# Kernel tuning notes

Measured on AMD Instinct MI355X. Metric: run time of the kernel, lower is better.

The kernel has to match this reference:

```python
import jax, jax.numpy as jnp
import numpy as np

B, S, D, E = 8, 4096, 4096, 64
CAP_FACTOR = 1.1


def setup_inputs() -> dict:
    key = jax.random.key(0)
    k1, k2 = jax.random.split(key)
    x = jax.random.normal(k1, (B, S, D), jnp.float32)
    # original zero-inits the router weight (degenerate routing); use small random
    # weights so top-2 routing is non-trivial. Forward math is identical.
    W = jax.random.normal(k2, (E, D), jnp.float32) * 0.02
    return {"x": x, "W": W}


def reference(x, W):
    b, s, d = x.shape
    e = W.shape[0]
    tokens = b * s
    capacity = int(tokens * CAP_FACTOR * 2 / e)  # static Python int

    # router: logits = x @ W^T (nn.Linear, no bias)
    logits = jnp.einsum('bsd,ed->bse', x, W)
    probs = jax.nn.softmax(logits, axis=-1)

    top2_p, top2_i = jax.lax.top_k(probs, 2)            # [b,s,2]
    top2_pn = top2_p / top2_p.sum(-1, keepdims=True)     # renormalized top-2 probs

    # Flatten the (token, slot) pairs in the same (i,j,k) enumeration order as
    # the reference triple loop; stable argsort reproduces its tie-breaking.
    n2 = tokens * 2
    e_flat = top2_i.reshape(n2)                          # expert id per slot
    p_flat = top2_pn.reshape(n2)                         # prob per slot
    onehot = e_flat[:, None] == jnp.arange(e)[None, :]   # [n2, e] bool

    # per-expert rank of each assigned slot by descending prob (stable)
    pe = jnp.where(onehot, p_flat[:, None], -jnp.inf)    # [n2, e]
    order = jnp.argsort(-pe, axis=0)                     # stable sort, desc prob
    rank = jnp.argsort(order, axis=0)                    # rank of slot within expert
    keep = onehot & (rank < capacity)                    # capacity truncation

    keep = keep.reshape(b, s, 2, e)
    dispatch = keep.any(axis=2).astype(x.dtype)                       # [b,s,e]
    combine = (keep.astype(x.dtype) * top2_pn[..., None]).sum(axis=2)  # [b,s,e]

    # aux loss: uses pre-truncation counts (expert_counts in the loop counts all
    # top-2 assignments, before capacity dropping)
    prob_per_expert = probs.sum(axis=(0, 1)) / tokens
    counts = onehot.sum(axis=0).astype(x.dtype)
    usage = counts / counts.sum()
    aux_loss = (prob_per_expert * usage).sum() * e

    return dispatch, combine, probs, aux_loss
```

## Files before the change

kernel.cpp:

```cpp
#include <hip/hip_runtime.h>
#include <hip/hip_bf16.h>
#include <cstdint>
#include <cstddef>

#define TOKENS   32768
#define DDIM     4096
#define NEXP     64
#define N2       65536
#define CAPACITY 1126

#define WS_WT    0
#define WS_PFLAT (1u << 20)
#define WS_EFLAT ((1u << 20) + 262144u)
#define WS_PSUM  ((1u << 20) + 524288u)
#define WS_CNT   ((1u << 20) + 524288u + 256u)

__global__ void zero_kernel(float* __restrict__ dc, float* __restrict__ psum) {
    int idx = blockIdx.x * blockDim.x + threadIdx.x;
    float4 z = make_float4(0.f, 0.f, 0.f, 0.f);
    const int n4 = (2 * TOKENS * NEXP) / 4;
    for (int i = idx; i < n4; i += gridDim.x * blockDim.x)
        ((float4*)dc)[i] = z;
    if (idx < NEXP) psum[idx] = 0.f;
}

__global__ void transpose_w(const float* __restrict__ W, float* __restrict__ Wt) {
    int idx = blockIdx.x * 256 + threadIdx.x;
    int d = idx >> 6, e = idx & 63;
    Wt[idx] = W[(size_t)e * DDIM + d];
}

__launch_bounds__(256, 2)
__global__ void router_kernel(const float* __restrict__ x, const float* __restrict__ Wt,
                              float* __restrict__ probs_out, float* __restrict__ p_flat,
                              int* __restrict__ e_flat, float* __restrict__ psum) {
    __shared__ __align__(16) float xs[64][68];
    __shared__ __align__(16) float wt[64][68];
    __shared__ __align__(16) float prow[64][68];
    __shared__ float red[256];

    const int tid  = threadIdx.x;
    const int tok0 = blockIdx.x * 64;
    const int ty4  = (tid >> 4) * 4;
    const int tx4  = (tid & 15) * 4;

    float tacc[4][4];
#pragma unroll
    for (int i = 0; i < 4; ++i)
#pragma unroll
        for (int j = 0; j < 4; ++j) tacc[i][j] = 0.f;

    for (int d0 = 0; d0 < DDIM; d0 += 64) {
        __syncthreads();
#pragma unroll
        for (int it = 0; it < 4; ++it) {
            int q   = it * 256 + tid;
            int row = q >> 4;
            int fp  = (q & 15) * 4;
            float4 xv = *(const float4*)&x[(size_t)(tok0 + row) * DDIM + d0 + fp];
            *(float4*)&xs[row][fp] = xv;
            float4 wv = *(const float4*)&Wt[(size_t)(d0 + row) * 64 + fp];
            *(float4*)&wt[row][fp] = wv;
        }
        __syncthreads();

        float cacc[4][4];
#pragma unroll
        for (int i = 0; i < 4; ++i)
#pragma unroll
            for (int j = 0; j < 4; ++j) cacc[i][j] = 0.f;

#pragma unroll 4
        for (int kk = 0; kk < 64; kk += 4) {
            float xr[4][4], wr[4][4];
#pragma unroll
            for (int i = 0; i < 4; ++i)
                *(float4*)xr[i] = *(const float4*)&xs[ty4 + i][kk];
#pragma unroll
            for (int t = 0; t < 4; ++t)
                *(float4*)wr[t] = *(const float4*)&wt[kk + t][tx4];
#pragma unroll
            for (int i = 0; i < 4; ++i)
#pragma unroll
                for (int t = 0; t < 4; ++t)
#pragma unroll
                    for (int j = 0; j < 4; ++j)
                        cacc[i][j] = fmaf(xr[i][t], wr[t][j], cacc[i][j]);
        }
#pragma unroll
        for (int i = 0; i < 4; ++i)
#pragma unroll
            for (int j = 0; j < 4; ++j) tacc[i][j] += cacc[i][j];
    }

    __syncthreads();
#pragma unroll
    for (int i = 0; i < 4; ++i)
        *(float4*)&prow[ty4 + i][tx4] =
            make_float4(tacc[i][0], tacc[i][1], tacc[i][2], tacc[i][3]);
    __syncthreads();

    if (tid < 64) {
        const int t = tid;
        float m = -INFINITY;
        for (int e = 0; e < 64; ++e) m = fmaxf(m, prow[t][e]);
        float s = 0.f;
        for (int e = 0; e < 64; ++e) {
            float v = expf(prow[t][e] - m);
            prow[t][e] = v;
            s += v;
        }
        float p1 = -1.f, p2 = -1.f; int i1 = 0, i2 = 0;
        for (int e = 0; e < 64; ++e) {
            float p = prow[t][e] / s;
            prow[t][e] = p;
            if (p > p1)      { p2 = p1; i2 = i1; p1 = p; i1 = e; }
            else if (p > p2) { p2 = p;  i2 = e; }
        }
        float rs  = p1 + p2;
        float pn1 = p1 / rs, pn2 = p2 / rs;
        int g = tok0 + t;
        p_flat[2 * g]     = pn1;
        p_flat[2 * g + 1] = pn2;
        e_flat[2 * g]     = i1;
        e_flat[2 * g + 1] = i2;
    }
    __syncthreads();

    float acc = 0.f;
#pragma unroll
    for (int k = 0; k < 16; ++k) {
        int idx = k * 256 + tid;
        int tok = idx >> 6, e = idx & 63;
        float p = prow[tok][e];
        probs_out[(size_t)(tok0 + tok) * 64 + e] = p;
        acc += p;
    }
    red[tid] = acc;
    __syncthreads();
    if (tid < 64) {
        float v = red[tid] + red[tid + 64] + red[tid + 128] + red[tid + 192];
        atomicAdd(&psum[tid], v);
    }
}

__launch_bounds__(256, 2)
__global__ void expert_sort_kernel(const float* __restrict__ p_flat,
                                   const int* __restrict__ e_flat,
                                   float* __restrict__ dispatch,
                                   float* __restrict__ combine,
                                   int* __restrict__ counts) {
    __shared__ unsigned long long keys[4096];
    __shared__ int cnt;
    const int tid = threadIdx.x;
    const int e   = blockIdx.x;

    if (tid == 0) cnt = 0;
    __syncthreads();

    for (int slot = tid; slot < N2; slot += 256) {
        if (e_flat[slot] == e) {
            float p = p_flat[slot];
            int pos = atomicAdd(&cnt, 1);
            if (pos < 4096)
                keys[pos] = ((unsigned long long)__float_as_uint(p) << 32) |
                            (unsigned long long)(0xFFFFFFFFu - (unsigned)slot);
        }
    }
    __syncthreads();
    const int n = cnt;
    for (int i = tid; i < 4096; i += 256)
        if (i >= n) keys[i] = 0ull;
    __syncthreads();

    for (int k = 2; k <= 4096; k <<= 1) {
        for (int j = k >> 1; j > 0; j >>= 1) {
#pragma unroll
            for (int w = 0; w < 16; ++w) {
                int i   = w * 256 + tid;
                int ixj = i ^ j;
                if (ixj > i) {
                    bool desc = ((i & k) == 0);
                    unsigned long long a = keys[i], b = keys[ixj];
                    bool sw = desc ? (a < b) : (a > b);
                    if (sw) { keys[i] = b; keys[ixj] = a; }
                }
            }
            __syncthreads();
        }
    }

    int lim = n < CAPACITY ? n : CAPACITY;
    for (int pos = tid; pos < lim; pos += 256) {
        unsigned long long key = keys[pos];
        unsigned slot = 0xFFFFFFFFu - (unsigned)(key & 0xFFFFFFFFull);
        float p = __uint_as_float((unsigned)(key >> 32));
        int token = (int)(slot >> 1);
        dispatch[(size_t)token * 64 + e] = 1.0f;
        combine [(size_t)token * 64 + e] = p;
    }
    if (tid == 0) counts[e] = n;
}

__global__ void aux_kernel(const float* __restrict__ psum,
                           const int* __restrict__ counts,
                           float* __restrict__ out_aux) {
    int tid = threadIdx.x;
    float v = (psum[tid] / (float)TOKENS) * ((float)counts[tid] / (float)N2);
    for (int off = 32; off > 0; off >>= 1) v += __shfl_down(v, off, 64);
    if (tid == 0) *out_aux = v * (float)NEXP;
}

extern "C" void kernel_launch(void* const* d_in, const int* in_sizes, int n_in,
                              void* d_out, int out_size, void* d_ws, size_t ws_size,
                              hipStream_t stream) {
    (void)in_sizes; (void)n_in; (void)out_size; (void)ws_size;

    const float* x = (const float*)d_in[0];
    const float* W = (const float*)d_in[1];

    float* out      = (float*)d_out;
    float* dispatch = out;
    float* combine  = out + (size_t)TOKENS * NEXP;
    float* probs    = out + (size_t)2 * TOKENS * NEXP;
    float* aux      = out + (size_t)3 * TOKENS * NEXP;

    char*  ws     = (char*)d_ws;
    float* Wt     = (float*)(ws + WS_WT);
    float* p_flat = (float*)(ws + WS_PFLAT);
    int*   e_flat = (int*)  (ws + WS_EFLAT);
    float* psum   = (float*)(ws + WS_PSUM);
    int*   counts = (int*)  (ws + WS_CNT);

    zero_kernel<<<1024, 256, 0, stream>>>(dispatch, psum);
    transpose_w<<<1024, 256, 0, stream>>>(W, Wt);
    router_kernel<<<512, 256, 0, stream>>>(x, Wt, probs, p_flat, e_flat, psum);
    expert_sort_kernel<<<64, 256, 0, stream>>>(p_flat, e_flat, dispatch, combine, counts);
    aux_kernel<<<1, 64, 0, stream>>>(psum, counts, aux);
}
```

Baseline: 1.029 ms.

## Split router GEMM over D with per-thread token rows and skip unneeded expert sorts

Replaces the shared-memory tiled router GEMM with a split-K kernel. Each thread computes all 64 logits for one token over one eighth of D, reading W directly with block-uniform addresses, so the separate W transpose kernel goes away. A new combine kernel reduces the 8 partial-sum slices and does the softmax, top-2 selection and probs write over 128 tokens per block. The expert sort now runs only when an expert's assignment count exceeds capacity, since otherwise every entry is kept and order does not matter; it also scans e_flat with vectorized int4 loads. The cost is a 64MB workspace of partials that must be written and read back, and heavy register use per thread.

```diff
diff --git a/kernel.cpp b/kernel.cpp
--- a/kernel.cpp
+++ b/kernel.cpp
@@ -8,12 +8,14 @@
 #define NEXP     64
 #define N2       65536
 #define CAPACITY 1126
-
-#define WS_WT    0
-#define WS_PFLAT (1u << 20)
-#define WS_EFLAT ((1u << 20) + 262144u)
-#define WS_PSUM  ((1u << 20) + 524288u)
-#define WS_CNT   ((1u << 20) + 524288u + 256u)
+#define DSPLIT   8
+#define DPART    (DDIM / DSPLIT)
+
+#define WS_PART  0
+#define WS_PFLAT (64u << 20)
+#define WS_EFLAT ((64u << 20) + 262144u)
+#define WS_PSUM  ((64u << 20) + 524288u)
+#define WS_CNT   ((64u << 20) + 524288u + 256u)
 
 __global__ void zero_kernel(float* __restrict__ dc, float* __restrict__ psum) {
     int idx = blockIdx.x * blockDim.x + threadIdx.x;
@@ -24,117 +26,117 @@
     if (idx < NEXP) psum[idx] = 0.f;
 }
 
-__global__ void transpose_w(const float* __restrict__ W, float* __restrict__ Wt) {
-    int idx = blockIdx.x * 256 + threadIdx.x;
-    int d = idx >> 6, e = idx & 63;
-    Wt[idx] = W[(size_t)e * DDIM + d];
-}
-
 __launch_bounds__(256, 2)
-__global__ void router_kernel(const float* __restrict__ x, const float* __restrict__ Wt,
-                              float* __restrict__ probs_out, float* __restrict__ p_flat,
-                              int* __restrict__ e_flat, float* __restrict__ psum) {
-    __shared__ __align__(16) float xs[64][68];
-    __shared__ __align__(16) float wt[64][68];
-    __shared__ __align__(16) float prow[64][68];
+__global__ void gemm_partial(const float* __restrict__ x, const float* __restrict__ W,
+                             float* __restrict__ part) {
+    const int tid = threadIdx.x;
+    const int dh  = blockIdx.x & (DSPLIT - 1);
+    const int tg  = blockIdx.x >> 3;
+    const int t   = tg * 256 + tid;
+    const float* xrow = x + (size_t)t * DDIM + dh * DPART;
+    const float* wq   = W + dh * DPART;
+
+    float tot[64];
+#pragma unroll
+    for (int e = 0; e < 64; ++e) tot[e] = 0.f;
+
+    for (int c = 0; c < DPART; c += 32) {
+        float xr[32];
+#pragma unroll
+        for (int j = 0; j < 32; j += 4) {
+            float4 v = *(const float4*)&xrow[c + j];
+            xr[j] = v.x; xr[j+1] = v.y; xr[j+2] = v.z; xr[j+3] = v.w;
+        }
+#pragma unroll
+        for (int e = 0; e < 64; ++e) {
+            const float* wrow = wq + (size_t)e * DDIM + c;
+            float s0 = 0.f, s1 = 0.f;
+#pragma unroll
+            for (int j = 0; j < 32; j += 2) {
+                s0 = fmaf(xr[j],     wrow[j],     s0);
+                s1 = fmaf(xr[j + 1], wrow[j + 1], s1);
+            }
+            tot[e] += (s0 + s1);
+        }
+    }
+    float* o = part + ((size_t)dh * TOKENS + t) * 64;
+#pragma unroll
+    for (int e = 0; e < 64; e += 4)
+        *(float4*)&o[e] = make_float4(tot[e], tot[e+1], tot[e+2], tot[e+3]);
+}
+
+__launch_bounds__(256, 2)
+__global__ void combine_kernel(const float* __restrict__ part,
+                               float* __restrict__ probs_out,
+                               float* __restrict__ p_flat,
+                               int* __restrict__ e_flat,
+                               float* __restrict__ psum) {
+    __shared__ __align__(16) float L[128][68];
     __shared__ float red[256];
-
     const int tid  = threadIdx.x;
-    const int tok0 = blockIdx.x * 64;
-    const int ty4  = (tid >> 4) * 4;
-    const int tx4  = (tid & 15) * 4;
-
-    float tacc[4][4];
-#pragma unroll
-    for (int i = 0; i < 4; ++i)
-#pragma unroll
-        for (int j = 0; j < 4; ++j) tacc[i][j] = 0.f;
-
-    for (int d0 = 0; d0 < DDIM; d0 += 64) {
-        __syncthreads();
-#pragma unroll
-        for (int it = 0; it < 4; ++it) {
-            int q   = it * 256 + tid;
-            int row = q >> 4;
-            int fp  = (q & 15) * 4;
-            float4 xv = *(const float4*)&x[(size_t)(tok0 + row) * DDIM + d0 + fp];
-            *(float4*)&xs[row][fp] = xv;
-            float4 wv = *(const float4*)&Wt[(size_t)(d0 + row) * 64 + fp];
-            *(float4*)&wt[row][fp] = wv;
-        }
-        __syncthreads();
-
-        float cacc[4][4];
-#pragma unroll
-        for (int i = 0; i < 4; ++i)
-#pragma unroll
-            for (int j = 0; j < 4; ++j) cacc[i][j] = 0.f;
-
-#pragma unroll 4
-        for (int kk = 0; kk < 64; kk += 4) {
-            float xr[4][4], wr[4][4];
-#pragma unroll
-            for (int i = 0; i < 4; ++i)
-                *(float4*)xr[i] = *(const float4*)&xs[ty4 + i][kk];
-#pragma unroll
-            for (int t = 0; t < 4; ++t)
-                *(float4*)wr[t] = *(const float4*)&wt[kk + t][tx4];
-#pragma unroll
-            for (int i = 0; i < 4; ++i)
-#pragma unroll
-                for (int t = 0; t < 4; ++t)
-#pragma unroll
-                    for (int j = 0; j < 4; ++j)
-                        cacc[i][j] = fmaf(xr[i][t], wr[t][j], cacc[i][j]);
-        }
-#pragma unroll
-        for (int i = 0; i < 4; ++i)
-#pragma unroll
-            for (int j = 0; j < 4; ++j) tacc[i][j] += cacc[i][j];
-    }
-
-    __syncthreads();
-#pragma unroll
-    for (int i = 0; i < 4; ++i)
-        *(float4*)&prow[ty4 + i][tx4] =
-            make_float4(tacc[i][0], tacc[i][1], tacc[i][2], tacc[i][3]);
-    __syncthreads();
-
-    if (tid < 64) {
+    const int tok0 = blockIdx.x * 128;
+    const size_t base = (size_t)tok0 * 64;
+
+#pragma unroll
+    for (int i = 0; i < 8; ++i) {
+        int idx4 = i * 256 + tid;
+        const float4* p0 = (const float4*)(part + 0ull * TOKENS * 64 + base) + idx4;
+        const float4* p1 = (const float4*)(part + 1ull * TOKENS * 64 + base) + idx4;
+        const float4* p2 = (const float4*)(part + 2ull * TOKENS * 64 + base) + idx4;
+        const float4* p3 = (const float4*)(part + 3ull * TOKENS * 64 + base) + idx4;
+        const float4* p4 = (const float4*)(part + 4ull * TOKENS * 64 + base) + idx4;
+        const float4* p5 = (const float4*)(part + 5ull * TOKENS * 64 + base) + idx4;
+        const float4* p6 = (const float4*)(part + 6ull * TOKENS * 64 + base) + idx4;
+        const float4* p7 = (const float4*)(part + 7ull * TOKENS * 64 + base) + idx4;
+        float4 a0 = *p0, a1 = *p1, a2 = *p2, a3 = *p3, a4 = *p4, a5 = *p5, a6 = *p6, a7 = *p7;
+        float4 s;
+        s.x = ((a0.x + a1.x) + (a2.x + a3.x)) + ((a4.x + a5.x) + (a6.x + a7.x));
+        s.y = ((a0.y + a1.y) + (a2.y + a3.y)) + ((a4.y + a5.y) + (a6.y + a7.y));
+        s.z = ((a0.z + a1.z) + (a2.z + a3.z)) + ((a4.z + a5.z) + (a6.z + a7.z));
+        s.w = ((a0.w + a1.w) + (a2.w + a3.w)) + ((a4.w + a5.w) + (a6.w + a7.w));
+        int row = idx4 >> 4, col = (idx4 & 15) * 4;
+        *(float4*)&L[row][col] = s;
+    }
+    __syncthreads();
+
+    if (tid < 128) {
         const int t = tid;
         float m = -INFINITY;
-        for (int e = 0; e < 64; ++e) m = fmaxf(m, prow[t][e]);
+#pragma unroll
+        for (int e = 0; e < 64; ++e) m = fmaxf(m, L[t][e]);
         float s = 0.f;
+        float v[64];
+#pragma unroll
+        for (int e = 0; e < 64; ++e) { v[e] = expf(L[t][e] - m); s += v[e]; }
+        float p1 = -1.f, p2 = -1.f; int i1 = 0, i2 = 0;
+#pragma unroll
         for (int e = 0; e < 64; ++e) {
-            float v = expf(prow[t][e] - m);
-            prow[t][e] = v;
-            s += v;
-        }
-        float p1 = -1.f, p2 = -1.f; int i1 = 0, i2 = 0;
-        for (int e = 0; e < 64; ++e) {
-            float p = prow[t][e] / s;
-            prow[t][e] = p;
+            float p = v[e] / s;
+            L[t][e] = p;
             if (p > p1)      { p2 = p1; i2 = i1; p1 = p; i1 = e; }
             else if (p > p2) { p2 = p;  i2 = e; }
         }
-        float rs  = p1 + p2;
-        float pn1 = p1 / rs, pn2 = p2 / rs;
+        float rs = p1 + p2;
         int g = tok0 + t;
-        p_flat[2 * g]     = pn1;
-        p_flat[2 * g + 1] = pn2;
+        p_flat[2 * g]     = p1 / rs;
+        p_flat[2 * g + 1] = p2 / rs;
         e_flat[2 * g]     = i1;
         e_flat[2 * g + 1] = i2;
     }
     __syncthreads();
 
+#pragma unroll
+    for (int i = 0; i < 8; ++i) {
+        int idx4 = i * 256 + tid;
+        int row = idx4 >> 4, col = (idx4 & 15) * 4;
+        ((float4*)(probs_out + base))[idx4] = *(const float4*)&L[row][col];
+    }
+
     float acc = 0.f;
-#pragma unroll
-    for (int k = 0; k < 16; ++k) {
-        int idx = k * 256 + tid;
-        int tok = idx >> 6, e = idx & 63;
-        float p = prow[tok][e];
-        probs_out[(size_t)(tok0 + tok) * 64 + e] = p;
-        acc += p;
+    {
+        int e = tid & 63, rg = (tid >> 6) * 32;
+#pragma unroll
+        for (int r = 0; r < 32; ++r) acc += L[rg + r][e];
     }
     red[tid] = acc;
     __syncthreads();
@@ -158,35 +160,44 @@
     if (tid == 0) cnt = 0;
     __syncthreads();
 
-    for (int slot = tid; slot < N2; slot += 256) {
-        if (e_flat[slot] == e) {
-            float p = p_flat[slot];
-            int pos = atomicAdd(&cnt, 1);
-            if (pos < 4096)
-                keys[pos] = ((unsigned long long)__float_as_uint(p) << 32) |
-                            (unsigned long long)(0xFFFFFFFFu - (unsigned)slot);
+    for (int i4 = tid; i4 < N2 / 4; i4 += 256) {
+        int4 ev = ((const int4*)e_flat)[i4];
+        int slot = i4 * 4;
+#pragma unroll
+        for (int j = 0; j < 4; ++j) {
+            int ee = (j == 0) ? ev.x : (j == 1) ? ev.y : (j == 2) ? ev.z : ev.w;
+            if (ee == e) {
+                float p = p_flat[slot + j];
+                int pos = atomicAdd(&cnt, 1);
+                if (pos < 4096)
+                    keys[pos] = ((unsigned long long)__float_as_uint(p) << 32) |
+                                (unsigned long long)(0xFFFFFFFFu - (unsigned)(slot + j));
+            }
         }
     }
     __syncthreads();
     const int n = cnt;
-    for (int i = tid; i < 4096; i += 256)
-        if (i >= n) keys[i] = 0ull;
-    __syncthreads();
-
-    for (int k = 2; k <= 4096; k <<= 1) {
-        for (int j = k >> 1; j > 0; j >>= 1) {
-#pragma unroll
-            for (int w = 0; w < 16; ++w) {
-                int i   = w * 256 + tid;
-                int ixj = i ^ j;
-                if (ixj > i) {
-                    bool desc = ((i & k) == 0);
-                    unsigned long long a = keys[i], b = keys[ixj];
-                    bool sw = desc ? (a < b) : (a > b);
-                    if (sw) { keys[i] = b; keys[ixj] = a; }
+
+    if (n > CAPACITY) {
+        int m = 2048;
+        while (m < n) m <<= 1;
+        for (int i = tid; i < m; i += 256)
+            if (i >= n) keys[i] = 0ull;
+        __syncthreads();
+
+        for (int k = 2; k <= m; k <<= 1) {
+            for (int j = k >> 1; j > 0; j >>= 1) {
+                for (int i = tid; i < m; i += 256) {
+                    int ixj = i ^ j;
+                    if (ixj > i) {
+                        bool desc = ((i & k) == 0);
+                        unsigned long long a = keys[i], b = keys[ixj];
+                        bool sw = desc ? (a < b) : (a > b);
+                        if (sw) { keys[i] = b; keys[ixj] = a; }
+                    }
                 }
+                __syncthreads();
             }
-            __syncthreads();
         }
     }
 
@@ -226,15 +237,15 @@
     float* aux      = out + (size_t)3 * TOKENS * NEXP;
 
     char*  ws     = (char*)d_ws;
-    float* Wt     = (float*)(ws + WS_WT);
+    float* part   = (float*)(ws + WS_PART);
     float* p_flat = (float*)(ws + WS_PFLAT);
     int*   e_flat = (int*)  (ws + WS_EFLAT);
     float* psum   = (float*)(ws + WS_PSUM);
     int*   counts = (int*)  (ws + WS_CNT);
 
     zero_kernel<<<1024, 256, 0, stream>>>(dispatch, psum);
-    transpose_w<<<1024, 256, 0, stream>>>(W, Wt);
-    router_kernel<<<512, 256, 0, stream>>>(x, Wt, probs, p_flat, e_flat, psum);
+    gemm_partial<<<1024, 256, 0, stream>>>(x, W, part);
+    combine_kernel<<<256, 256, 0, stream>>>(part, probs, p_flat, e_flat, psum);
     expert_sort_kernel<<<64, 256, 0, stream>>>(p_flat, e_flat, dispatch, combine, counts);
     aux_kernel<<<1, 64, 0, stream>>>(psum, counts, aux);
 }
```

Result: slower. 1.250 ms (+21.5%).
